# Kernel tuning notes

Measured on AMD Instinct MI355X. Metric: run time of the kernel, lower is better.

## Reference

```python
import jax, jax.numpy as jnp
import numpy as np

B, S, D = 2, 2048, 1024
H, HD = 16, 64  # num heads, head dim
EPS = 1e-12
SCALING = HD ** -0.5


def rotate_half(x):
    x1, x2 = jnp.split(x, 2, axis=-1)
    return jnp.concatenate([-x2, x1], axis=-1)


def setup_inputs() -> dict:
    key = jax.random.key(0)
    ks = jax.random.split(key, 12)
    hidden_states = jax.random.normal(ks[0], (B, S, D), dtype=jnp.float32)
    # RoPE tables (standard rotate-half convention)
    inv_freq = 1.0 / (10000.0 ** (np.arange(0, HD, 2, dtype=np.float32) / HD))
    pos = np.arange(S, dtype=np.float32)
    freqs = np.outer(pos, inv_freq)  # [S, HD/2]
    emb = np.concatenate([freqs, freqs], axis=-1)  # [S, HD]
    cos = jnp.asarray(np.cos(emb))
    sin = jnp.asarray(np.sin(emb))
    w = 0.02
    return {
        "hidden_states": hidden_states,
        "cos": cos,
        "sin": sin,
        "Wq": jax.random.normal(ks[1], (D, D), dtype=jnp.float32) * w,
        "bq": jnp.zeros((D,), dtype=jnp.float32),
        "Wk": jax.random.normal(ks[2], (D, D), dtype=jnp.float32) * w,
        "bk": jnp.zeros((D,), dtype=jnp.float32),
        "Wv": jax.random.normal(ks[3], (D, D), dtype=jnp.float32) * w,
        "bv": jnp.zeros((D,), dtype=jnp.float32),
        "Wo": jax.random.normal(ks[4], (D, D), dtype=jnp.float32) * w,
        "bo": jnp.zeros((D,), dtype=jnp.float32),
        "ln_w": jnp.ones((D,), dtype=jnp.float32),
        "ln_b": jnp.zeros((D,), dtype=jnp.float32),
    }


def reference(hidden_states, cos, sin, Wq, bq, Wk, bk, Wv, bv, Wo, bo, ln_w, ln_b):
    b, s, d = hidden_states.shape
    # QKV projections -> [b, h, s, hd]
    def proj(W, bias):
        return (hidden_states @ W.T + bias).reshape(b, s, H, HD).transpose(0, 2, 1, 3)
    q, k, v = proj(Wq, bq), proj(Wk, bk), proj(Wv, bv)
    # RoPE (cos/sin broadcast over batch and head dims)
    c = cos[None, None, :, :]
    sn = sin[None, None, :, :]
    q = q * c + rotate_half(q) * sn
    k = k * c + rotate_half(k) * sn
    # Faithful to source: query pre-scaled AND scaling applied inside attention
    q = q * SCALING
    scores = jnp.einsum("bhsd,bhtd->bhst", q, k) * SCALING
    attn = jax.nn.softmax(scores, axis=-1)
    ctx = jnp.einsum("bhst,bhtd->bhsd", attn, v)  # [b,h,s,hd]
    ctx = ctx.transpose(0, 2, 1, 3).reshape(b, s, d)
    # output dense + residual + LayerNorm
    out = ctx @ Wo.T + bo + hidden_states
    mu = jnp.mean(out, axis=-1, keepdims=True)
    var = jnp.var(out, axis=-1, keepdims=True)
    return (out - mu) / jnp.sqrt(var + EPS) * ln_w + ln_b
```

## Files before the change

kernel.cpp:

```cpp
#include <hip/hip_runtime.h>
#include <hip/hip_bf16.h>
#include <stdint.h>


typedef unsigned short ushort_t;
typedef short bf16x8 __attribute__((ext_vector_type(8)));
typedef float f32x4 __attribute__((ext_vector_type(4)));
typedef float f32x16 __attribute__((ext_vector_type(16)));
typedef unsigned short ushort8 __attribute__((ext_vector_type(8)));

#define LOG2E 1.4426950408889634f

__device__ __forceinline__ ushort_t f2b(float f) {
  uint32_t x = __builtin_bit_cast(uint32_t, f);
  return (ushort_t)((x + 0x7FFFu + ((x >> 16) & 1u)) >> 16);
}

__device__ __forceinline__ uint32_t cvt_pk_bf16(float lo, float hi) {
  uint32_t r;
  asm("v_cvt_pk_bf16_f32 %0, %1, %2" : "=v"(r) : "v"(lo), "v"(hi));
  return r;
}

__device__ __forceinline__ void permswap(uint32_t& a, uint32_t& b) {
  asm volatile("v_permlane32_swap_b32 %0, %1" : "+v"(a), "+v"(b));
}

__device__ __forceinline__ void gload16(const void* gptr, void* ldsptr) {
  __builtin_amdgcn_global_load_lds(
      (const __attribute__((address_space(1))) uint32_t*)gptr,
      (__attribute__((address_space(3))) uint32_t*)ldsptr, 16, 0, 0);
}

__global__ void cast_all_kernel(const float* __restrict__ h,
                                const float* __restrict__ a, const float* __restrict__ b,
                                const float* __restrict__ c, const float* __restrict__ d2,
                                ushort_t* __restrict__ oh, ushort_t* __restrict__ oa,
                                ushort_t* __restrict__ ob, ushort_t* __restrict__ oc,
                                ushort_t* __restrict__ od) {
  const int blk = blockIdx.x;
  const float* src;
  ushort_t* dst;
  int rel;
  if (blk < 2048) { src = h; dst = oh; rel = blk; }
  else {
    const int w = (blk - 2048) >> 9;
    rel = (blk - 2048) & 511;
    src = w == 0 ? a : w == 1 ? b : w == 2 ? c : d2;
    dst = w == 0 ? oa : w == 1 ? ob : w == 2 ? oc : od;
  }
  const int i = (rel * 256 + threadIdx.x) * 8;
  const float4* s = (const float4*)(src + i);
  float4 x = s[0], y = s[1];
  ushort8 o = { f2b(x.x), f2b(x.y), f2b(x.z), f2b(x.w),
                f2b(y.x), f2b(y.y), f2b(y.z), f2b(y.w) };
  *(ushort8*)(dst + i) = o;
}

__global__ __launch_bounds__(256) void gemm_qkv(
    const ushort_t* __restrict__ hid, const ushort_t* __restrict__ wq,
    const ushort_t* __restrict__ wk, const ushort_t* __restrict__ wv,
    const float* __restrict__ bq, const float* __restrict__ bk,
    const float* __restrict__ bv, const float* __restrict__ cosT,
    const float* __restrict__ sinT, ushort_t* __restrict__ qout,
    ushort_t* __restrict__ kout, ushort_t* __restrict__ vtout)
{
  constexpr int K = 1024;
  __shared__ uint4 SB[3072];
  const int which = blockIdx.z;
  const ushort_t* A;
  const ushort_t* Bm;
  const float* bias;
  int m0, n0;
  if (which == 0)      { A = hid; Bm = wq; bias = bq; m0 = blockIdx.x * 128; n0 = blockIdx.y * 128; }
  else if (which == 1) { A = hid; Bm = wk; bias = bk; m0 = blockIdx.x * 128; n0 = blockIdx.y * 128; }
  else                 { A = wv;  Bm = hid; bias = bv; m0 = blockIdx.y * 128; n0 = blockIdx.x * 128; }

  const int tid = threadIdx.x;
  const int wave = tid >> 6, lane = tid & 63;
  const int d = lane & 15, g = lane >> 4;
  const int wm = (wave >> 1) * 64, wn = (wave & 1) * 64;

  const ushort_t* ag = A + (size_t)(m0 + (tid >> 2)) * K + (tid & 3) * 8;
  const ushort_t* bg = Bm + (size_t)(n0 + (tid >> 2)) * K + (tid & 3) * 8;

  f32x4 acc[4][4] = {};

#define STAGE_Q(buf, k0)                                           \
  {                                                                \
    char* dst = (char*)SB + (buf) * 16384 + wave * 1024;           \
    gload16(ag + (k0), dst);                                       \
    gload16(ag + 64 * K + (k0), dst + 4096);                       \
    gload16(bg + (k0), dst + 8192);                                \
    gload16(bg + 64 * K + (k0), dst + 12288);                      \
  }

#define COMPUTE_Q(buf)                                                          \
  {                                                                             \
    bf16x8 af[4], bfr[4];                                                       \
    _Pragma("unroll") for (int i = 0; i < 4; ++i)                               \
        af[i] = __builtin_bit_cast(bf16x8,                                      \
            SB[(buf) * 1024 + (wm + i * 16 + d) * 4 + g]);                      \
    _Pragma("unroll") for (int j = 0; j < 4; ++j)                               \
        bfr[j] = __builtin_bit_cast(bf16x8,                                     \
            SB[(buf) * 1024 + 512 + (wn + j * 16 + d) * 4 + g]);                \
    _Pragma("unroll") for (int i = 0; i < 4; ++i)                               \
        _Pragma("unroll") for (int j = 0; j < 4; ++j)                           \
            acc[i][j] = __builtin_amdgcn_mfma_f32_16x16x32_bf16(                \
                af[i], bfr[j], acc[i][j], 0, 0, 0);                             \
  }

  STAGE_Q(0, 0);
  STAGE_Q(1, 32);
  asm volatile("s_waitcnt vmcnt(4)" ::: "memory");
  __builtin_amdgcn_s_barrier();

  int bufc = 0;
  for (int t = 0; t < 30; ++t) {
    int bufn = bufc + 2; if (bufn >= 3) bufn -= 3;
    STAGE_Q(bufn, (t + 2) * 32);
    COMPUTE_Q(bufc);
    asm volatile("s_waitcnt vmcnt(4)" ::: "memory");
    __builtin_amdgcn_s_barrier();
    bufc = (bufc == 2) ? 0 : bufc + 1;
  }
  COMPUTE_Q(bufc);
  asm volatile("s_waitcnt vmcnt(0)" ::: "memory");
  __builtin_amdgcn_s_barrier();
  bufc = (bufc == 2) ? 0 : bufc + 1;
  COMPUTE_Q(bufc);
#undef STAGE_Q
#undef COMPUTE_Q

  if (which <= 1) {
    ushort_t* O = which == 0 ? qout : kout;
    const float qscale = which == 0 ? (LOG2E / 64.0f) : 1.0f;
    const int head_base = n0 + wn;
    const int h = head_base >> 6;
#pragma unroll
    for (int i = 0; i < 4; ++i) {
#pragma unroll
      for (int r = 0; r < 4; ++r) {
        const int m = m0 + wm + i * 16 + g * 4 + r;
        const int s = m & 2047, b = m >> 11;
#pragma unroll
        for (int j = 0; j < 4; ++j) {
          const int c = j * 16 + d;
          const float v0 = acc[i][j][r] + bias[head_base + c];
          const float v1 = acc[i][j ^ 2][r] + bias[head_base + (c ^ 32)];
          const float rot = (c < 32) ? -v1 : v1;
          const float vr = (v0 * cosT[s * 64 + c] + rot * sinT[s * 64 + c]) * qscale;
          O[(size_t)(((b << 4) + h) * 2048 + s) * 64 + c] = f2b(vr);
        }
      }
    }
  } else {
    ushort_t* O = vtout;
#pragma unroll
    for (int i = 0; i < 4; ++i) {
#pragma unroll
      for (int r = 0; r < 4; ++r) {
        const int fr = m0 + wm + i * 16 + g * 4 + r;
        const float bv2 = bias[fr];
        const int h = fr >> 6, dd = fr & 63;
#pragma unroll
        for (int j = 0; j < 4; ++j) {
          const int tok = n0 + wn + j * 16 + d;
          const int b = tok >> 11, s = tok & 2047;
          O[(size_t)(((b << 4) + h) * 64 + dd) * 2048 + s] = f2b(acc[i][j][r] + bv2);
        }
      }
    }
  }
}

__global__ __launch_bounds__(256) void gemm_wo(
    const ushort_t* __restrict__ A, const ushort_t* __restrict__ B,
    const float* __restrict__ bias, const float* __restrict__ resid,
    float* __restrict__ O)
{
  constexpr int K = 1024;
  __shared__ uint4 SB[3072];
  const int tid = threadIdx.x;
  const int wave = tid >> 6, lane = tid & 63;
  const int d = lane & 15, g = lane >> 4;
  const int m0 = blockIdx.x * 128, n0 = blockIdx.y * 128;
  const int wm = (wave >> 1) * 64, wn = (wave & 1) * 64;

  const ushort_t* ag = A + (size_t)(m0 + (tid >> 2)) * K + (tid & 3) * 8;
  const ushort_t* bg = B + (size_t)(n0 + (tid >> 2)) * K + (tid & 3) * 8;

  f32x4 acc[4][4] = {};

#define STAGE_W(buf, k0)                                           \
  {                                                                \
    char* dst = (char*)SB + (buf) * 16384 + wave * 1024;           \
    gload16(ag + (k0), dst);                                       \
    gload16(ag + 64 * K + (k0), dst + 4096);                       \
    gload16(bg + (k0), dst + 8192);                                \
    gload16(bg + 64 * K + (k0), dst + 12288);                      \
  }

#define COMPUTE_W(buf)                                                          \
  {                                                                             \
    bf16x8 af[4], bfr[4];                                                       \
    _Pragma("unroll") for (int i = 0; i < 4; ++i)                               \
        af[i] = __builtin_bit_cast(bf16x8,                                      \
            SB[(buf) * 1024 + (wm + i * 16 + d) * 4 + g]);                      \
    _Pragma("unroll") for (int j = 0; j < 4; ++j)                               \
        bfr[j] = __builtin_bit_cast(bf16x8,                                     \
            SB[(buf) * 1024 + 512 + (wn + j * 16 + d) * 4 + g]);                \
    _Pragma("unroll") for (int i = 0; i < 4; ++i)                               \
        _Pragma("unroll") for (int j = 0; j < 4; ++j)                           \
            acc[i][j] = __builtin_amdgcn_mfma_f32_16x16x32_bf16(                \
                af[i], bfr[j], acc[i][j], 0, 0, 0);                             \
  }

  STAGE_W(0, 0);
  STAGE_W(1, 32);
  asm volatile("s_waitcnt vmcnt(4)" ::: "memory");
  __builtin_amdgcn_s_barrier();

  int bufc = 0;
  for (int t = 0; t < 30; ++t) {
    int bufn = bufc + 2; if (bufn >= 3) bufn -= 3;
    STAGE_W(bufn, (t + 2) * 32);
    COMPUTE_W(bufc);
    asm volatile("s_waitcnt vmcnt(4)" ::: "memory");
    __builtin_amdgcn_s_barrier();
    bufc = (bufc == 2) ? 0 : bufc + 1;
  }
  COMPUTE_W(bufc);
  asm volatile("s_waitcnt vmcnt(0)" ::: "memory");
  __builtin_amdgcn_s_barrier();
  bufc = (bufc == 2) ? 0 : bufc + 1;
  COMPUTE_W(bufc);
#undef STAGE_W
#undef COMPUTE_W

#pragma unroll
  for (int i = 0; i < 4; ++i)
#pragma unroll
    for (int r = 0; r < 4; ++r) {
      const int m = m0 + wm + i * 16 + g * 4 + r;
#pragma unroll
      for (int j = 0; j < 4; ++j) {
        const int n = n0 + wn + j * 16 + d;
        O[(size_t)m * 1024 + n] = acc[i][j][r] + bias[n] + resid[(size_t)m * 1024 + n];
      }
    }
}

__global__ __launch_bounds__(512) void attn_kernel(
    const ushort_t* __restrict__ Q, const ushort_t* __restrict__ Kb,
    const ushort_t* __restrict__ VT, ushort_t* __restrict__ ctx)
{
  __shared__ uint4 KV[2048];
  __shared__ float Ls[256];
  const int orig = blockIdx.x;
  const int wgid = (orig & 7) * 64 + (orig >> 3);
  const int bh = wgid >> 4;
  const int q0 = (wgid & 15) * 128;
  const int tid = threadIdx.x;
  const int wave = tid >> 6, lane = tid & 63;
  const int qw = wave >> 1, half = wave & 1;
  const int ql = lane & 31, h2 = lane >> 5;
  const int qrow = q0 + qw * 32 + ql;

  bf16x8 qf[4];
  {
    const ushort_t* qp = Q + ((size_t)bh * 2048 + qrow) * 64 + h2 * 8;
#pragma unroll
    for (int s = 0; s < 4; ++s)
      qf[s] = __builtin_bit_cast(bf16x8, *(const uint4*)(qp + 16 * s));
  }

  bf16x8 onesf;
  {
    uint4 ou = {0x3F803F80u, 0x3F803F80u, 0x3F803F80u, 0x3F803F80u};
    onesf = __builtin_bit_cast(bf16x8, ou);
  }

  const int st_row = tid >> 3, st_c8 = tid & 7;
  const ushort_t* kgp = Kb + (size_t)(bh * 2048 + st_row) * 64 + st_c8 * 8;
  const ushort_t* vgp = VT + (size_t)(bh * 64 + st_row) * 2048 + st_c8 * 8;
  const int sidx = st_row * 8 + (st_c8 ^ (st_row & 7));

  uint4 kr = *(const uint4*)(kgp);
  uint4 vr = *(const uint4*)(vgp);
  KV[sidx] = kr;
  KV[512 + sidx] = vr;
  __syncthreads();

  f32x16 cacc[2] = {};
  f32x16 lacc = {};

#define ATT_COMPUTE(CB)                                                         \
  {                                                                             \
    f32x16 z = {};                                                              \
    _Pragma("unroll") for (int s = 0; s < 4; ++s) {                             \
      bf16x8 kf = __builtin_bit_cast(bf16x8,                                    \
          KV[(CB) + (half * 32 + ql) * 8 + ((2 * s + h2) ^ (ql & 7))]);         \
      z = __builtin_amdgcn_mfma_f32_32x32x16_bf16(kf, qf[s], z, 0, 0, 0);       \
    }                                                                           \
    bf16x8 pf[2];                                                               \
    _Pragma("unroll") for (int s2 = 0; s2 < 2; ++s2) {                          \
      const int rb = s2 * 8;                                                    \
      float p0 = __builtin_amdgcn_exp2f(z[rb + 0]);                             \
      float p1 = __builtin_amdgcn_exp2f(z[rb + 1]);                             \
      float p2 = __builtin_amdgcn_exp2f(z[rb + 2]);                             \
      float p3 = __builtin_amdgcn_exp2f(z[rb + 3]);                             \
      float p4 = __builtin_amdgcn_exp2f(z[rb + 4]);                             \
      float p5 = __builtin_amdgcn_exp2f(z[rb + 5]);                             \
      float p6 = __builtin_amdgcn_exp2f(z[rb + 6]);                             \
      float p7 = __builtin_amdgcn_exp2f(z[rb + 7]);                             \
      uint32_t a1 = cvt_pk_bf16(p0, p1);                                        \
      uint32_t a2 = cvt_pk_bf16(p2, p3);                                        \
      uint32_t b1 = cvt_pk_bf16(p4, p5);                                        \
      uint32_t b2 = cvt_pk_bf16(p6, p7);                                        \
      permswap(a1, b1);                                                         \
      permswap(a2, b2);                                                         \
      uint4 u = {a1, a2, b1, b2};                                               \
      pf[s2] = __builtin_bit_cast(bf16x8, u);                                   \
    }                                                                           \
    _Pragma("unroll") for (int s2 = 0; s2 < 2; ++s2)                            \
      lacc = __builtin_amdgcn_mfma_f32_32x32x16_bf16(onesf, pf[s2], lacc,       \
                                                     0, 0, 0);                  \
    _Pragma("unroll") for (int dt = 0; dt < 2; ++dt)                            \
      _Pragma("unroll") for (int s2 = 0; s2 < 2; ++s2) {                        \
        const int s = 2 * half + s2;                                            \
        bf16x8 vf = __builtin_bit_cast(bf16x8,                                  \
            KV[(CB) + 512 + (dt * 32 + ql) * 8 + ((2 * s + h2) ^ (ql & 7))]);   \
        cacc[dt] = __builtin_amdgcn_mfma_f32_32x32x16_bf16(vf, pf[s2],          \
                                                           cacc[dt], 0, 0, 0); \
      }                                                                         \
  }

  const ushort_t* kP = kgp + 4096;
  const ushort_t* vP = vgp + 64;
  for (int tt = 0; tt < 16; ++tt) {
    kr = *(const uint4*)(kP);
    vr = *(const uint4*)(vP);
    ATT_COMPUTE(0)
    KV[1024 + sidx] = kr;
    KV[1536 + sidx] = vr;
    __syncthreads();
    if (tt < 15) {
      kr = *(const uint4*)(kP + 4096);
      vr = *(const uint4*)(vP + 64);
    }
    ATT_COMPUTE(1024)
    if (tt < 15) {
      KV[sidx] = kr;
      KV[512 + sidx] = vr;
      __syncthreads();
    }
    kP += 8192;
    vP += 128;
  }
#undef ATT_COMPUTE

  float lsum = lacc[0];

  __syncthreads();
  float* Lf = (float*)KV;
  const int slot = qw * 64 + lane;
  if (half == 1) {
#pragma unroll
    for (int dt = 0; dt < 2; ++dt)
#pragma unroll
      for (int r = 0; r < 16; ++r)
        Lf[slot * 32 + ((dt * 16 + r) ^ (lane & 31))] = cacc[dt][r];
    Ls[slot] = lsum;
  }
  __syncthreads();
  if (half == 0) {
#pragma unroll
    for (int dt = 0; dt < 2; ++dt)
#pragma unroll
      for (int r = 0; r < 16; ++r)
        cacc[dt][r] += Lf[slot * 32 + ((dt * 16 + r) ^ (lane & 31))];
    lsum += Ls[slot];

    const float rinv = 1.0f / lsum;
    const int b = bh >> 4, h = bh & 15;
    ushort_t* cp = ctx + ((size_t)(b * 2048 + qrow)) * 1024 + h * 64 + h2 * 4;
#pragma unroll
    for (int dt = 0; dt < 2; ++dt)
#pragma unroll
      for (int t = 0; t < 4; ++t) {
        uint2 w;
        w.x = cvt_pk_bf16(cacc[dt][4 * t + 0] * rinv, cacc[dt][4 * t + 1] * rinv);
        w.y = cvt_pk_bf16(cacc[dt][4 * t + 2] * rinv, cacc[dt][4 * t + 3] * rinv);
        *(uint2*)(cp + dt * 32 + t * 8) = w;
      }
  }
}

__global__ __launch_bounds__(256) void ln_kernel(const float* __restrict__ x,
    const float* __restrict__ w, const float* __restrict__ b2, float* __restrict__ out)
{
  const int row = blockIdx.x, tid = threadIdx.x;
  const float4 v = ((const float4*)(x + (size_t)row * 1024))[tid];
  float s = v.x + v.y + v.z + v.w;
  float ss = v.x * v.x + v.y * v.y + v.z * v.z + v.w * v.w;
#pragma unroll
  for (int off = 32; off > 0; off >>= 1) {
    s += __shfl_down(s, off, 64);
    ss += __shfl_down(ss, off, 64);
  }
  __shared__ float red[8];
  if ((tid & 63) == 0) { red[tid >> 6] = s; red[4 + (tid >> 6)] = ss; }
  __syncthreads();
  const float S = red[0] + red[1] + red[2] + red[3];
  const float SS = red[4] + red[5] + red[6] + red[7];
  const float mu = S * (1.f / 1024.f);
  const float rstd = rsqrtf(SS * (1.f / 1024.f) - mu * mu + 1e-12f);
  const int c = tid * 4;
  float4 o;
  o.x = (v.x - mu) * rstd * w[c + 0] + b2[c + 0];
  o.y = (v.y - mu) * rstd * w[c + 1] + b2[c + 1];
  o.z = (v.z - mu) * rstd * w[c + 2] + b2[c + 2];
  o.w = (v.w - mu) * rstd * w[c + 3] + b2[c + 3];
  ((float4*)(out + (size_t)row * 1024))[tid] = o;
}

extern "C" void kernel_launch(void* const* d_in, const int* in_sizes, int n_in,
                              void* d_out, int out_size, void* d_ws, size_t ws_size,
                              hipStream_t stream) {
  const float* hidden = (const float*)d_in[0];
  const float* cosT = (const float*)d_in[1];
  const float* sinT = (const float*)d_in[2];
  const float* Wq = (const float*)d_in[3];
  const float* bq = (const float*)d_in[4];
  const float* Wk = (const float*)d_in[5];
  const float* bk = (const float*)d_in[6];
  const float* Wv = (const float*)d_in[7];
  const float* bv = (const float*)d_in[8];
  const float* Wo = (const float*)d_in[9];
  const float* bo = (const float*)d_in[10];
  const float* lnw = (const float*)d_in[11];
  const float* lnb = (const float*)d_in[12];

  char* ws = (char*)d_ws;
  const size_t MB = 1u << 20;
  ushort_t* hid_bf = (ushort_t*)(ws);
  ushort_t* wq_bf = (ushort_t*)(ws + 8 * MB);
  ushort_t* wk_bf = (ushort_t*)(ws + 10 * MB);
  ushort_t* wv_bf = (ushort_t*)(ws + 12 * MB);
  ushort_t* wo_bf = (ushort_t*)(ws + 14 * MB);
  ushort_t* q_buf = (ushort_t*)(ws + 16 * MB);
  ushort_t* k_buf = (ushort_t*)(ws + 24 * MB);
  ushort_t* vt_buf = (ushort_t*)(ws + 32 * MB);
  ushort_t* ctx_bf = (ushort_t*)(ws + 40 * MB);
  float* out_pre = (float*)(ws + 16 * MB);

  cast_all_kernel<<<4096, 256, 0, stream>>>(hidden, Wq, Wk, Wv, Wo,
                                            hid_bf, wq_bf, wk_bf, wv_bf, wo_bf);

  gemm_qkv<<<dim3(32, 8, 3), 256, 0, stream>>>(hid_bf, wq_bf, wk_bf, wv_bf,
                                               bq, bk, bv, cosT, sinT,
                                               q_buf, k_buf, vt_buf);
  attn_kernel<<<512, 512, 0, stream>>>(q_buf, k_buf, vt_buf, ctx_bf);
  gemm_wo<<<dim3(32, 8), 256, 0, stream>>>(ctx_bf, wo_bf, bo, hidden, out_pre);
  ln_kernel<<<4096, 256, 0, stream>>>(out_pre, lnw, lnb, (float*)d_out);
}
```

Before: 109.4 us.

## Enlarge GEMM tiles to 256x128 with 8 waves per block

The QKV and output-projection GEMMs now use 512-thread blocks that each compute a 256x128 tile instead of 128x128. The B tile in shared memory is shared across twice as many rows, so per-thread global loads drop from four to three per stage and grid size halves. The V-projection block index mapping is remapped to the new tile shape. This reduces B-operand reload traffic but halves the number of blocks, which may lower occupancy and wave-level parallelism on a many-CU device.

```diff
diff --git a/kernel.cpp b/kernel.cpp
--- a/kernel.cpp
+++ b/kernel.cpp
@@ -57,7 +57,7 @@
   *(ushort8*)(dst + i) = o;
 }
 
-__global__ __launch_bounds__(256) void gemm_qkv(
+__global__ __launch_bounds__(512) void gemm_qkv(
     const ushort_t* __restrict__ hid, const ushort_t* __restrict__ wq,
     const ushort_t* __restrict__ wk, const ushort_t* __restrict__ wv,
     const float* __restrict__ bq, const float* __restrict__ bk,
@@ -66,15 +66,18 @@
     ushort_t* __restrict__ kout, ushort_t* __restrict__ vtout)
 {
   constexpr int K = 1024;
-  __shared__ uint4 SB[3072];
+  __shared__ uint4 SBa[3072];
+  __shared__ uint4 SBb[1536];
   const int which = blockIdx.z;
   const ushort_t* A;
   const ushort_t* Bm;
   const float* bias;
   int m0, n0;
-  if (which == 0)      { A = hid; Bm = wq; bias = bq; m0 = blockIdx.x * 128; n0 = blockIdx.y * 128; }
-  else if (which == 1) { A = hid; Bm = wk; bias = bk; m0 = blockIdx.x * 128; n0 = blockIdx.y * 128; }
-  else                 { A = wv;  Bm = hid; bias = bv; m0 = blockIdx.y * 128; n0 = blockIdx.x * 128; }
+  if (which == 0)      { A = hid; Bm = wq; bias = bq; m0 = blockIdx.x * 256; n0 = blockIdx.y * 128; }
+  else if (which == 1) { A = hid; Bm = wk; bias = bk; m0 = blockIdx.x * 256; n0 = blockIdx.y * 128; }
+  else                 { A = wv;  Bm = hid; bias = bv;
+                         m0 = (blockIdx.y & 3) * 256;
+                         n0 = (blockIdx.x + (blockIdx.y >> 2) * 16) * 128; }
 
   const int tid = threadIdx.x;
   const int wave = tid >> 6, lane = tid & 63;
@@ -88,11 +91,11 @@
 
 #define STAGE_Q(buf, k0)                                           \
   {                                                                \
-    char* dst = (char*)SB + (buf) * 16384 + wave * 1024;           \
-    gload16(ag + (k0), dst);                                       \
-    gload16(ag + 64 * K + (k0), dst + 4096);                       \
-    gload16(bg + (k0), dst + 8192);                                \
-    gload16(bg + 64 * K + (k0), dst + 12288);                      \
+    char* da = (char*)(SBa + (buf) * 1024) + wave * 1024;          \
+    char* db = (char*)(SBb + (buf) * 512) + wave * 1024;           \
+    gload16(ag + (k0), da);                                        \
+    gload16(ag + 128 * K + (k0), da + 8192);                       \
+    gload16(bg + (k0), db);                                        \
   }
 
 #define COMPUTE_Q(buf)                                                          \
@@ -100,10 +103,10 @@
     bf16x8 af[4], bfr[4];                                                       \
     _Pragma("unroll") for (int i = 0; i < 4; ++i)                               \
         af[i] = __builtin_bit_cast(bf16x8,                                      \
-            SB[(buf) * 1024 + (wm + i * 16 + d) * 4 + g]);                      \
+            SBa[(buf) * 1024 + (wm + i * 16 + d) * 4 + g]);                     \
     _Pragma("unroll") for (int j = 0; j < 4; ++j)                               \
         bfr[j] = __builtin_bit_cast(bf16x8,                                     \
-            SB[(buf) * 1024 + 512 + (wn + j * 16 + d) * 4 + g]);                \
+            SBb[(buf) * 512 + (wn + j * 16 + d) * 4 + g]);                      \
     _Pragma("unroll") for (int i = 0; i < 4; ++i)                               \
         _Pragma("unroll") for (int j = 0; j < 4; ++j)                           \
             acc[i][j] = __builtin_amdgcn_mfma_f32_16x16x32_bf16(                \
@@ -112,7 +115,7 @@
 
   STAGE_Q(0, 0);
   STAGE_Q(1, 32);
-  asm volatile("s_waitcnt vmcnt(4)" ::: "memory");
+  asm volatile("s_waitcnt vmcnt(3)" ::: "memory");
   __builtin_amdgcn_s_barrier();
 
   int bufc = 0;
@@ -120,7 +123,7 @@
     int bufn = bufc + 2; if (bufn >= 3) bufn -= 3;
     STAGE_Q(bufn, (t + 2) * 32);
     COMPUTE_Q(bufc);
-    asm volatile("s_waitcnt vmcnt(4)" ::: "memory");
+    asm volatile("s_waitcnt vmcnt(3)" ::: "memory");
     __builtin_amdgcn_s_barrier();
     bufc = (bufc == 2) ? 0 : bufc + 1;
   }
@@ -174,17 +177,18 @@
   }
 }
 
-__global__ __launch_bounds__(256) void gemm_wo(
+__global__ __launch_bounds__(512) void gemm_wo(
     const ushort_t* __restrict__ A, const ushort_t* __restrict__ B,
     const float* __restrict__ bias, const float* __restrict__ resid,
     float* __restrict__ O)
 {
   constexpr int K = 1024;
-  __shared__ uint4 SB[3072];
+  __shared__ uint4 SBa[3072];
+  __shared__ uint4 SBb[1536];
   const int tid = threadIdx.x;
   const int wave = tid >> 6, lane = tid & 63;
   const int d = lane & 15, g = lane >> 4;
-  const int m0 = blockIdx.x * 128, n0 = blockIdx.y * 128;
+  const int m0 = blockIdx.x * 256, n0 = blockIdx.y * 128;
   const int wm = (wave >> 1) * 64, wn = (wave & 1) * 64;
 
   const ushort_t* ag = A + (size_t)(m0 + (tid >> 2)) * K + (tid & 3) * 8;
@@ -194,11 +198,11 @@
 
 #define STAGE_W(buf, k0)                                           \
   {                                                                \
-    char* dst = (char*)SB + (buf) * 16384 + wave * 1024;           \
-    gload16(ag + (k0), dst);                                       \
-    gload16(ag + 64 * K + (k0), dst + 4096);                       \
-    gload16(bg + (k0), dst + 8192);                                \
-    gload16(bg + 64 * K + (k0), dst + 12288);                      \
+    char* da = (char*)(SBa + (buf) * 1024) + wave * 1024;          \
+    char* db = (char*)(SBb + (buf) * 512) + wave * 1024;           \
+    gload16(ag + (k0), da);                                        \
+    gload16(ag + 128 * K + (k0), da + 8192);                       \
+    gload16(bg + (k0), db);                                        \
   }
 
 #define COMPUTE_W(buf)                                                          \
@@ -206,10 +210,10 @@
     bf16x8 af[4], bfr[4];                                                       \
     _Pragma("unroll") for (int i = 0; i < 4; ++i)                               \
         af[i] = __builtin_bit_cast(bf16x8,                                      \
-            SB[(buf) * 1024 + (wm + i * 16 + d) * 4 + g]);                      \
+            SBa[(buf) * 1024 + (wm + i * 16 + d) * 4 + g]);                     \
     _Pragma("unroll") for (int j = 0; j < 4; ++j)                               \
         bfr[j] = __builtin_bit_cast(bf16x8,                                     \
-            SB[(buf) * 1024 + 512 + (wn + j * 16 + d) * 4 + g]);                \
+            SBb[(buf) * 512 + (wn + j * 16 + d) * 4 + g]);                      \
     _Pragma("unroll") for (int i = 0; i < 4; ++i)                               \
         _Pragma("unroll") for (int j = 0; j < 4; ++j)                           \
             acc[i][j] = __builtin_amdgcn_mfma_f32_16x16x32_bf16(                \
@@ -218,7 +222,7 @@
 
   STAGE_W(0, 0);
   STAGE_W(1, 32);
-  asm volatile("s_waitcnt vmcnt(4)" ::: "memory");
+  asm volatile("s_waitcnt vmcnt(3)" ::: "memory");
   __builtin_amdgcn_s_barrier();
 
   int bufc = 0;
@@ -226,7 +230,7 @@
     int bufn = bufc + 2; if (bufn >= 3) bufn -= 3;
     STAGE_W(bufn, (t + 2) * 32);
     COMPUTE_W(bufc);
-    asm volatile("s_waitcnt vmcnt(4)" ::: "memory");
+    asm volatile("s_waitcnt vmcnt(3)" ::: "memory");
     __builtin_amdgcn_s_barrier();
     bufc = (bufc == 2) ? 0 : bufc + 1;
   }
@@ -458,10 +462,10 @@
   cast_all_kernel<<<4096, 256, 0, stream>>>(hidden, Wq, Wk, Wv, Wo,
                                             hid_bf, wq_bf, wk_bf, wv_bf, wo_bf);
 
-  gemm_qkv<<<dim3(32, 8, 3), 256, 0, stream>>>(hid_bf, wq_bf, wk_bf, wv_bf,
+  gemm_qkv<<<dim3(16, 8, 3), 512, 0, stream>>>(hid_bf, wq_bf, wk_bf, wv_bf,
                                                bq, bk, bv, cosT, sinT,
                                                q_buf, k_buf, vt_buf);
   attn_kernel<<<512, 512, 0, stream>>>(q_buf, k_buf, vt_buf, ctx_bf);
-  gemm_wo<<<dim3(32, 8), 256, 0, stream>>>(ctx_bf, wo_bf, bo, hidden, out_pre);
+  gemm_wo<<<dim3(16, 8), 512, 0, stream>>>(ctx_bf, wo_bf, bo, hidden, out_pre);
   ln_kernel<<<4096, 256, 0, stream>>>(out_pre, lnw, lnb, (float*)d_out);
 }
```

After: 125.7 us. 1.15x slower.
